# Performance work log

Hardware: AMD Instinct MI355X
Metric: run time of the kernel (lower is better)

Reference implementation:

```python
import jax, jax.numpy as jnp
import numpy as np

K = 3
NUM_STEP_COMBO = 5
BN_EPS = 1e-5


def setup_inputs() -> dict:
    key = jax.random.key(0)
    ks = jax.random.split(key, 10)
    N, E, D, H, O, G = 100000, 1600000, 48, 128, 12, 64
    x = jax.random.normal(ks[0], (N, D), dtype=jnp.float32)
    edge_index = jax.random.randint(ks[1], (2, E), 0, N, dtype=jnp.int64)
    batch = jnp.sort(jax.random.randint(ks[2], (N,), 0, G, dtype=jnp.int64))
    # ChebConv params: one [D, D] weight per Chebyshev order, shared bias
    W = jax.random.normal(ks[3], (K, D, D), dtype=jnp.float32) * 0.1
    b = jnp.zeros((D,), dtype=jnp.float32)
    gamma = jnp.ones((D,), dtype=jnp.float32)
    beta = jnp.zeros((D,), dtype=jnp.float32)
    W1 = jax.random.normal(ks[4], (D, H), dtype=jnp.float32) * 0.1
    b1 = jnp.zeros((H,), dtype=jnp.float32)
    W2 = jax.random.normal(ks[5], (H, O), dtype=jnp.float32) * 0.1
    b2 = jnp.zeros((O,), dtype=jnp.float32)
    return {"x": x, "edge_index": edge_index, "batch": batch, "num_graphs": 64,
            "W": W, "b": b, "gamma": gamma, "beta": beta,
            "W1": W1, "b1": b1, "W2": W2, "b2": b2}


def cheb_conv(x, row, col, W, b):
    # PyG ChebConv, sym norm, lambda_max=2 => L_hat = -D^{-1/2} A D^{-1/2}
    N = x.shape[0]
    deg = jax.ops.segment_sum(jnp.ones_like(row, dtype=x.dtype), row, num_segments=N)
    dinv = jnp.where(deg > 0, jax.lax.rsqrt(jnp.maximum(deg, 1.0)), 0.0)
    norm = (-dinv[row] * dinv[col])[:, None]  # [E,1] edge weights of L_hat

    def lhat(v):  # sparse matvec: gather neighbors, scale, scatter-add
        return jax.ops.segment_sum(norm * v[col], row, num_segments=N)

    Tx0 = x
    Tx1 = lhat(x)
    out = Tx0 @ W[0] + Tx1 @ W[1]
    Txkm2, Txkm1 = Tx0, Tx1
    for k in range(2, W.shape[0]):
        Txk = 2.0 * lhat(Txkm1) - Txkm2
        out = out + Txk @ W[k]
        Txkm2, Txkm1 = Txkm1, Txk
    return out + b


def reference(x, edge_index, batch, num_graphs, W, b, gamma, beta, W1, b1, W2, b2):
    row, col = edge_index[0], edge_index[1]
    N = x.shape[0]
    out = x
    for _ in range(NUM_STEP_COMBO):
        t = jax.nn.relu(cheb_conv(out, row, col, W, b))
        # BatchNorm1d (training-mode stats over all nodes, biased var)
        mean = jnp.mean(t, axis=0)
        var = jnp.mean((t - mean) ** 2, axis=0)
        t = gamma * (t - mean) * jax.lax.rsqrt(var + BN_EPS) + beta
        # graph_max_pool: per-node max over incoming neighbor features
        m = jax.ops.segment_max(t[col], row, num_segments=N)
        out = jnp.where(jnp.isneginf(m), 0.0, m)  # empty segments -> 0
    g = jax.ops.segment_sum(out, batch, num_segments=num_graphs)  # global_add_pool
    h = jax.nn.relu(g @ W1 + b1)
    return h @ W2 + b2
```

## Files before the change

### kernel.cpp

```cpp
#include <hip/hip_runtime.h>
#include <hip/hip_bf16.h>

#define D 48
#define RB 96
#define GNUM 64
#define HDIM 128
#define ODIM 12
#define BN_EPS 1e-5f

typedef _Float16 half4v __attribute__((ext_vector_type(4)));
typedef _Float16 half8v __attribute__((ext_vector_type(8)));
typedef float f32x4 __attribute__((ext_vector_type(4)));

#define MFMA16(a, b, c) __builtin_amdgcn_mfma_f32_16x16x16f16((a), (b), (c), 0, 0, 0)

__device__ __forceinline__ half8v h8max(half8v a, half8v b) {
    half8v r;
#pragma unroll
    for (int k = 0; k < 8; ++k) r[k] = a[k] > b[k] ? a[k] : b[k];
    return r;
}
__device__ __forceinline__ half8v h8min(half8v a, half8v b) {
    half8v r;
#pragma unroll
    for (int k = 0; k < 8; ++k) r[k] = a[k] < b[k] ? a[k] : b[k];
    return r;
}
__device__ __forceinline__ half8v h8shfl_xor(half8v v, int mask) {
    union { half8v h; int i[4]; } u;
    u.h = v;
#pragma unroll
    for (int k = 0; k < 4; ++k) u.i[k] = __shfl_xor(u.i[k], mask);
    return u.h;
}


__global__ __launch_bounds__(256) void k_deg(const int* __restrict__ row, int* __restrict__ deg, int E) {
    int e = blockIdx.x * 256 + threadIdx.x;
    if (e < E) atomicAdd(&deg[row[e]], 1);
}

__global__ __launch_bounds__(256) void k_scan1(const int* __restrict__ deg, int* __restrict__ incl,
                                               int* __restrict__ bsum, float* __restrict__ dinv, int N) {
    __shared__ int s[256];
    int i = blockIdx.x * 256 + threadIdx.x;
    int d = (i < N) ? deg[i] : 0;
    if (i < N) dinv[i] = d > 0 ? rsqrtf((float)d) : 0.f;
    s[threadIdx.x] = d;
    __syncthreads();
    for (int off = 1; off < 256; off <<= 1) {
        int t = (threadIdx.x >= off) ? s[threadIdx.x - off] : 0;
        __syncthreads();
        s[threadIdx.x] += t;
        __syncthreads();
    }
    if (i < N) incl[i] = s[threadIdx.x];
    if (threadIdx.x == 255) bsum[blockIdx.x] = s[255];
}

__global__ __launch_bounds__(512) void k_scan2(int* __restrict__ bsum, int nb) {
    __shared__ int s[512];
    int t = threadIdx.x;
    s[t] = (t < nb) ? bsum[t] : 0;
    __syncthreads();
    for (int off = 1; off < 512; off <<= 1) {
        int v = (t >= off) ? s[t - off] : 0;
        __syncthreads();
        s[t] += v;
        __syncthreads();
    }
    if (t < nb) bsum[t] = s[t];
}

__global__ __launch_bounds__(256) void k_scan3(const int* __restrict__ incl, const int* __restrict__ bsum,
                                               int* __restrict__ rowptr, int N) {
    int i = blockIdx.x * 256 + threadIdx.x;
    if (i < N) {
        int add = (blockIdx.x > 0) ? bsum[blockIdx.x - 1] : 0;
        rowptr[i + 1] = incl[i] + add;
    }
    if (i == 0) rowptr[0] = 0;
}

__global__ __launch_bounds__(256) void k_fill(const int* __restrict__ row, const int* __restrict__ col,
                                              const int* __restrict__ rowptr, int* __restrict__ fillc,
                                              const float* __restrict__ dinv, int2* __restrict__ epair,
                                              int e0, int e1, int N) {
    int part = blockIdx.x & 7;
    int sub = blockIdx.x >> 3;
    int nsub = (int)(gridDim.x >> 3);
    int lo = (int)(((long long)N * part) >> 3);
    int hi = (int)(((long long)N * (part + 1)) >> 3);
    for (int e = e0 + sub * 256 + threadIdx.x; e < e1; e += nsub * 256) {
        int r = row[e];
        if (r >= lo && r < hi) {
            int c = col[e];
            int p = rowptr[r] + atomicAdd(&fillc[r], 1);
            epair[p] = make_int2(c * RB, __float_as_int(dinv[c]));
        }
    }
}

__global__ __launch_bounds__(256) void k_cvt(const float* __restrict__ x, _Float16* __restrict__ xh, int n4) {
    int i = blockIdx.x * 256 + threadIdx.x;
    if (i < n4) {
        float4 v = ((const float4*)x)[i];
        half4v h;
        h.x = (_Float16)v.x; h.y = (_Float16)v.y; h.z = (_Float16)v.z; h.w = (_Float16)v.w;
        ((half4v*)xh)[i] = h;
    }
}

__global__ __launch_bounds__(256) void k_wb(const float* __restrict__ W, _Float16* __restrict__ WB) {
    int idx = blockIdx.x * 256 + threadIdx.x;
    if (idx < 27 * 64) {
        int lane = idx & 63, ct = idx >> 6;
        int c = ct / 3, tl = ct % 3;
        int col = lane & 15, kg = lane >> 4;
        half4v h;
#pragma unroll
        for (int j = 0; j < 4; ++j) h[j] = (_Float16)W[(c * 16 + kg * 4 + j) * 48 + tl * 16 + col];
        *(half4v*)(WB + (size_t)idx * 4) = h;
    }
}


#define GATHER_REDUCE8(A)                                             \
    A##0 += __shfl_xor(A##0, 8);  A##1 += __shfl_xor(A##1, 8);        \
    A##2 += __shfl_xor(A##2, 8);  A##3 += __shfl_xor(A##3, 8);        \
    A##4 += __shfl_xor(A##4, 8);  A##5 += __shfl_xor(A##5, 8);        \
    A##6 += __shfl_xor(A##6, 8);  A##7 += __shfl_xor(A##7, 8);        \
    A##0 += __shfl_xor(A##0, 16); A##1 += __shfl_xor(A##1, 16);       \
    A##2 += __shfl_xor(A##2, 16); A##3 += __shfl_xor(A##3, 16);       \
    A##4 += __shfl_xor(A##4, 16); A##5 += __shfl_xor(A##5, 16);       \
    A##6 += __shfl_xor(A##6, 16); A##7 += __shfl_xor(A##7, 16);       \
    A##0 += __shfl_xor(A##0, 32); A##1 += __shfl_xor(A##1, 32);       \
    A##2 += __shfl_xor(A##2, 32); A##3 += __shfl_xor(A##3, 32);       \
    A##4 += __shfl_xor(A##4, 32); A##5 += __shfl_xor(A##5, 32);       \
    A##6 += __shfl_xor(A##6, 32); A##7 += __shfl_xor(A##7, 32);

__global__ __launch_bounds__(256) void k_lhat(const _Float16* __restrict__ cur, const int* __restrict__ rowptr,
                                              const int2* __restrict__ epair, const float* __restrict__ dinv,
                                              _Float16* __restrict__ tx1, int N) {
    int lane = threadIdx.x & 63;
    int i = (blockIdx.x * 256 + threadIdx.x) >> 6;
    if (i >= N) return;
    int slot = lane >> 3, j = lane & 7;
    int jbB = (j < 6 ? j : 5) * 16;
    const char* base = (const char*)cur + jbB;
    int s = rowptr[i], e = rowptr[i + 1];
    float a0 = 0.f, a1 = 0.f, a2 = 0.f, a3 = 0.f, a4 = 0.f, a5 = 0.f, a6 = 0.f, a7 = 0.f;
    int p = s + slot;
    for (; p + 8 < e; p += 16) {
        int2 ea = epair[p], eb = epair[p + 8];
        half8v ha = *(const half8v*)(base + (unsigned)ea.x);
        half8v hb = *(const half8v*)(base + (unsigned)eb.x);
        float wa = __int_as_float(ea.y), wb = __int_as_float(eb.y);
        a0 += wa * (float)ha[0] + wb * (float)hb[0];
        a1 += wa * (float)ha[1] + wb * (float)hb[1];
        a2 += wa * (float)ha[2] + wb * (float)hb[2];
        a3 += wa * (float)ha[3] + wb * (float)hb[3];
        a4 += wa * (float)ha[4] + wb * (float)hb[4];
        a5 += wa * (float)ha[5] + wb * (float)hb[5];
        a6 += wa * (float)ha[6] + wb * (float)hb[6];
        a7 += wa * (float)ha[7] + wb * (float)hb[7];
    }
    if (p < e) {
        int2 ea = epair[p];
        half8v ha = *(const half8v*)(base + (unsigned)ea.x);
        float wa = __int_as_float(ea.y);
        a0 += wa * (float)ha[0]; a1 += wa * (float)ha[1]; a2 += wa * (float)ha[2]; a3 += wa * (float)ha[3];
        a4 += wa * (float)ha[4]; a5 += wa * (float)ha[5]; a6 += wa * (float)ha[6]; a7 += wa * (float)ha[7];
    }
    GATHER_REDUCE8(a)
    if (slot == 0 && j < 6) {
        float sc = -dinv[i];
        half8v o;
        o[0] = (_Float16)(sc * a0); o[1] = (_Float16)(sc * a1);
        o[2] = (_Float16)(sc * a2); o[3] = (_Float16)(sc * a3);
        o[4] = (_Float16)(sc * a4); o[5] = (_Float16)(sc * a5);
        o[6] = (_Float16)(sc * a6); o[7] = (_Float16)(sc * a7);
        *(half8v*)((char*)tx1 + (size_t)i * RB + jbB) = o;
    }
}

__global__ __launch_bounds__(256) void k_gather2(const _Float16* __restrict__ tx0, const _Float16* __restrict__ tx1,
                                                 const int* __restrict__ rowptr, const int2* __restrict__ epair,
                                                 const float* __restrict__ dinv, _Float16* __restrict__ tx2, int N) {
    int lane = threadIdx.x & 63;
    int i = (blockIdx.x * 256 + threadIdx.x) >> 6;
    if (i >= N) return;
    int slot = lane >> 3, j = lane & 7;
    int jbB = (j < 6 ? j : 5) * 16;
    const char* base = (const char*)tx1 + jbB;
    int s = rowptr[i], e = rowptr[i + 1];
    float a0 = 0.f, a1 = 0.f, a2 = 0.f, a3 = 0.f, a4 = 0.f, a5 = 0.f, a6 = 0.f, a7 = 0.f;
    int p = s + slot;
    for (; p + 8 < e; p += 16) {
        int2 ea = epair[p], eb = epair[p + 8];
        half8v ha = *(const half8v*)(base + (unsigned)ea.x);
        half8v hb = *(const half8v*)(base + (unsigned)eb.x);
        float wa = __int_as_float(ea.y), wb = __int_as_float(eb.y);
        a0 += wa * (float)ha[0] + wb * (float)hb[0];
        a1 += wa * (float)ha[1] + wb * (float)hb[1];
        a2 += wa * (float)ha[2] + wb * (float)hb[2];
        a3 += wa * (float)ha[3] + wb * (float)hb[3];
        a4 += wa * (float)ha[4] + wb * (float)hb[4];
        a5 += wa * (float)ha[5] + wb * (float)hb[5];
        a6 += wa * (float)ha[6] + wb * (float)hb[6];
        a7 += wa * (float)ha[7] + wb * (float)hb[7];
    }
    if (p < e) {
        int2 ea = epair[p];
        half8v ha = *(const half8v*)(base + (unsigned)ea.x);
        float wa = __int_as_float(ea.y);
        a0 += wa * (float)ha[0]; a1 += wa * (float)ha[1]; a2 += wa * (float)ha[2]; a3 += wa * (float)ha[3];
        a4 += wa * (float)ha[4]; a5 += wa * (float)ha[5]; a6 += wa * (float)ha[6]; a7 += wa * (float)ha[7];
    }
    GATHER_REDUCE8(a)
    if (slot == 0 && j < 6) {
        float sc = -2.f * dinv[i];
        half8v h0 = *(const half8v*)((const char*)tx0 + (size_t)i * RB + jbB);
        half8v o;
        o[0] = (_Float16)(sc * a0 - (float)h0[0]); o[1] = (_Float16)(sc * a1 - (float)h0[1]);
        o[2] = (_Float16)(sc * a2 - (float)h0[2]); o[3] = (_Float16)(sc * a3 - (float)h0[3]);
        o[4] = (_Float16)(sc * a4 - (float)h0[4]); o[5] = (_Float16)(sc * a5 - (float)h0[5]);
        o[6] = (_Float16)(sc * a6 - (float)h0[6]); o[7] = (_Float16)(sc * a7 - (float)h0[7]);
        *(half8v*)((char*)tx2 + (size_t)i * RB + jbB) = o;
    }
}


__global__ __launch_bounds__(256) void k_dense(const _Float16* __restrict__ tx0, const _Float16* __restrict__ tx1,
                                               const _Float16* __restrict__ tx2, const _Float16* __restrict__ WB,
                                               const float* __restrict__ b, _Float16* __restrict__ tbuf,
                                               float* __restrict__ bnst, int N) {
    __shared__ float bns[2 * D];
    int t = threadIdx.x;
    if (t < 2 * D) bns[t] = 0.f;
    __syncthreads();

    int lane = t & 63, wave = t >> 6;
    int node0 = (blockIdx.x * 4 + wave) * 16;
    if (node0 < N) {
        int col = lane & 15, kg = lane >> 4;
        int nodeA = node0 + col;
        bool inA = nodeA < N;
        const _Float16* __restrict__ Xs[3] = {tx0 + (size_t)nodeA * D, tx1 + (size_t)nodeA * D,
                                              tx2 + (size_t)nodeA * D};
        f32x4 acc0 = {}, acc1 = {}, acc2 = {};
#pragma unroll
        for (int c = 0; c < 9; ++c) {
            half4v a = {};
            if (inA) a = *(const half4v*)(Xs[c / 3] + (c % 3) * 16 + kg * 4);
            half4v b0 = *(const half4v*)(WB + ((size_t)(c * 3 + 0) * 64 + lane) * 4);
            half4v b1 = *(const half4v*)(WB + ((size_t)(c * 3 + 1) * 64 + lane) * 4);
            half4v b2 = *(const half4v*)(WB + ((size_t)(c * 3 + 2) * 64 + lane) * 4);
            acc0 = MFMA16(a, b0, acc0);
            acc1 = MFMA16(a, b1, acc1);
            acc2 = MFMA16(a, b2, acc2);
        }
        float bc0 = b[col], bc1 = b[16 + col], bc2 = b[32 + col];
        float s0 = 0.f, q0 = 0.f, s1 = 0.f, q1 = 0.f, s2 = 0.f, q2 = 0.f;
#pragma unroll
        for (int i = 0; i < 4; ++i) {
            int nd = node0 + kg * 4 + i;
            float v0 = fmaxf(acc0[i] + bc0, 0.f);
            float v1 = fmaxf(acc1[i] + bc1, 0.f);
            float v2 = fmaxf(acc2[i] + bc2, 0.f);
            if (nd < N) {
                _Float16* o = tbuf + (size_t)nd * D;
                o[col] = (_Float16)v0;
                o[16 + col] = (_Float16)v1;
                o[32 + col] = (_Float16)v2;
                s0 += v0; q0 += v0 * v0;
                s1 += v1; q1 += v1 * v1;
                s2 += v2; q2 += v2 * v2;
            }
        }
        s0 += __shfl_xor(s0, 16); s0 += __shfl_xor(s0, 32);
        q0 += __shfl_xor(q0, 16); q0 += __shfl_xor(q0, 32);
        s1 += __shfl_xor(s1, 16); s1 += __shfl_xor(s1, 32);
        q1 += __shfl_xor(q1, 16); q1 += __shfl_xor(q1, 32);
        s2 += __shfl_xor(s2, 16); s2 += __shfl_xor(s2, 32);
        q2 += __shfl_xor(q2, 16); q2 += __shfl_xor(q2, 32);
        if (lane < 16) {
            atomicAdd(&bns[col], s0);      atomicAdd(&bns[D + col], q0);
            atomicAdd(&bns[16 + col], s1); atomicAdd(&bns[D + 16 + col], q1);
            atomicAdd(&bns[32 + col], s2); atomicAdd(&bns[D + 32 + col], q2);
        }
    }
    __syncthreads();
    if (t < 2 * D) atomicAdd(&bnst[t], bns[t]);
}


__global__ __launch_bounds__(256) void k_pool(const _Float16* __restrict__ tbuf, const int* __restrict__ rowptr,
                                              const int2* __restrict__ epair, const float* __restrict__ bnst,
                                              const float* __restrict__ gamma, const float* __restrict__ beta,
                                              float Ninv, _Float16* __restrict__ outh, int N) {
    __shared__ float ssL[2 * D];
    int t = threadIdx.x;
    if (t < D) {
        float mean = bnst[t] * Ninv;
        float var = fmaxf(bnst[D + t] * Ninv - mean * mean, 0.f);
        float sc = gamma[t] * rsqrtf(var + BN_EPS);
        ssL[t] = sc;
        ssL[D + t] = beta[t] - mean * sc;
    }
    __syncthreads();
    int lane = t & 63;
    int i = (blockIdx.x * 256 + t) >> 6;
    if (i >= N) return;
    int slot = lane >> 3, j = lane & 7;
    int jbB = (j < 6 ? j : 5) * 16;
    const char* base = (const char*)tbuf + jbB;
    int s = rowptr[i], e = rowptr[i + 1];
    half8v m, n;
#pragma unroll
    for (int k = 0; k < 8; ++k) { m[k] = (_Float16)(-60000.f); n[k] = (_Float16)(60000.f); }
    int p = s + slot;
    for (; p + 8 < e; p += 16) {
        int oa = epair[p].x, ob = epair[p + 8].x;
        half8v ha = *(const half8v*)(base + (unsigned)oa);
        half8v hb = *(const half8v*)(base + (unsigned)ob);
        m = h8max(m, h8max(ha, hb));
        n = h8min(n, h8min(ha, hb));
    }
    if (p < e) {
        half8v ha = *(const half8v*)(base + (unsigned)epair[p].x);
        m = h8max(m, ha);
        n = h8min(n, ha);
    }
    m = h8max(m, h8shfl_xor(m, 8));
    n = h8min(n, h8shfl_xor(n, 8));
    m = h8max(m, h8shfl_xor(m, 16));
    n = h8min(n, h8shfl_xor(n, 16));
    m = h8max(m, h8shfl_xor(m, 32));
    n = h8min(n, h8shfl_xor(n, 32));
    if (slot == 0 && j < 6) {
        int jb = (j < 6 ? j : 5) * 8;
        half8v o;
        if (s == e) {
#pragma unroll
            for (int k = 0; k < 8; ++k) o[k] = (_Float16)0.f;
        } else {
#pragma unroll
            for (int k = 0; k < 8; ++k) {
                float sc = ssL[jb + k], sh = ssL[D + jb + k];
                float v = (sc >= 0.f) ? sc * (float)m[k] + sh : sc * (float)n[k] + sh;
                o[k] = (_Float16)v;
            }
        }
        *(half8v*)((char*)outh + (size_t)i * RB + jbB) = o;
    }
}


__global__ __launch_bounds__(256) void k_gpool(const _Float16* __restrict__ outh, const int* __restrict__ batch,
                                               float* __restrict__ g, int N, int chunk) {
    int lane = threadIdx.x & 63;
    int wid = (blockIdx.x * 256 + threadIdx.x) >> 6;
    int start = wid * chunk;
    if (start >= N || lane >= 12) return;
    int end = start + chunk;
    if (end > N) end = N;
    int curb = batch[start];
    float a0 = 0.f, a1 = 0.f, a2 = 0.f, a3 = 0.f;
    for (int i = start; i < end; ++i) {
        int bi = batch[i];
        if (bi != curb) {
            atomicAdd(&g[curb * D + lane * 4 + 0], a0); atomicAdd(&g[curb * D + lane * 4 + 1], a1);
            atomicAdd(&g[curb * D + lane * 4 + 2], a2); atomicAdd(&g[curb * D + lane * 4 + 3], a3);
            curb = bi; a0 = a1 = a2 = a3 = 0.f;
        }
        half4v h = *(const half4v*)(outh + (size_t)i * D + lane * 4);
        a0 += (float)h.x; a1 += (float)h.y; a2 += (float)h.z; a3 += (float)h.w;
    }
    atomicAdd(&g[curb * D + lane * 4 + 0], a0); atomicAdd(&g[curb * D + lane * 4 + 1], a1);
    atomicAdd(&g[curb * D + lane * 4 + 2], a2); atomicAdd(&g[curb * D + lane * 4 + 3], a3);
}

__global__ __launch_bounds__(256) void k_mlp(const float* __restrict__ g, const float* __restrict__ W1,
                                             const float* __restrict__ b1, const float* __restrict__ W2,
                                             const float* __restrict__ b2, float* __restrict__ out) {
    __shared__ float gL[GNUM * D];
    __shared__ float hL[GNUM * HDIM];
    __shared__ float W1L[D * HDIM];
    int t = threadIdx.x;
    for (int i = t; i < GNUM * D; i += 256) gL[i] = g[i];
    for (int i = t; i < D * HDIM; i += 256) W1L[i] = W1[i];
    __syncthreads();
    for (int i = t; i < GNUM * HDIM; i += 256) {
        int gi = i >> 7, hj = i & 127;
        float a = b1[hj];
        for (int k = 0; k < D; ++k) a += gL[gi * D + k] * W1L[k * HDIM + hj];
        hL[i] = fmaxf(a, 0.f);
    }
    __syncthreads();
    for (int i = t; i < GNUM * ODIM; i += 256) {
        int gi = i / ODIM, oj = i % ODIM;
        float a = b2[oj];
        for (int k = 0; k < HDIM; ++k) a += hL[gi * HDIM + k] * W2[k * ODIM + oj];
        out[i] = a;
    }
}


extern "C" void kernel_launch(void* const* d_in, const int* in_sizes, int n_in,
                              void* d_out, int out_size, void* d_ws, size_t ws_size,
                              hipStream_t stream) {
    const float* x     = (const float*)d_in[0];
    const int*   ei    = (const int*)d_in[1];
    const int*   batch = (const int*)d_in[2];
    const float* W     = (const float*)d_in[4];
    const float* b     = (const float*)d_in[5];
    const float* gamma = (const float*)d_in[6];
    const float* beta  = (const float*)d_in[7];
    const float* W1    = (const float*)d_in[8];
    const float* b1    = (const float*)d_in[9];
    const float* W2    = (const float*)d_in[10];
    const float* b2    = (const float*)d_in[11];

    int N = in_sizes[0] / D;
    int E = in_sizes[1] / 2;
    const int* row = ei;
    const int* col = ei + E;

    char* w = (char*)d_ws;
    auto alloc = [&](size_t bytes) { char* p = w; w += (bytes + 255) & ~(size_t)255; return p; };
    int*       deg     = (int*)alloc((size_t)N * 4);
    float*     dinv    = (float*)alloc((size_t)N * 4);
    int*       fillc   = (int*)alloc((size_t)N * 4);
    int*       incl    = (int*)alloc((size_t)N * 4);
    int*       bsum    = (int*)alloc(4096);
    int*       rowptr  = (int*)alloc((size_t)(N + 1) * 4);
    int2*      epair   = (int2*)alloc((size_t)E * 8);
    _Float16*  xh      = (_Float16*)alloc((size_t)N * D * 2 + 64);
    _Float16*  tx1h    = (_Float16*)alloc((size_t)N * D * 2 + 64);
    _Float16*  tx2h    = (_Float16*)alloc((size_t)N * D * 2 + 64);
    _Float16*  tbufh   = (_Float16*)alloc((size_t)N * D * 2 + 64);
    _Float16*  outh    = (_Float16*)alloc((size_t)N * D * 2 + 64);
    _Float16*  WB      = (_Float16*)alloc(27 * 64 * 4 * 2);
    float*     bnstats = (float*)alloc(5 * 2 * D * 4);
    float*     g       = (float*)alloc((size_t)GNUM * D * 4);

    (void)hipMemsetAsync(deg, 0, (size_t)N * 4, stream);
    (void)hipMemsetAsync(fillc, 0, (size_t)N * 4, stream);
    (void)hipMemsetAsync(bnstats, 0, 5 * 2 * D * 4, stream);
    (void)hipMemsetAsync(g, 0, (size_t)GNUM * D * 4, stream);

    int nbE = (E + 255) / 256;
    int nbN = (N + 255) / 256;

    k_deg<<<nbE, 256, 0, stream>>>(row, deg, E);
    k_scan1<<<nbN, 256, 0, stream>>>(deg, incl, bsum, dinv, N);
    k_scan2<<<1, 512, 0, stream>>>(bsum, nbN);
    k_scan3<<<nbN, 256, 0, stream>>>(incl, bsum, rowptr, N);
    int E3 = E / 3;
    k_fill<<<2048, 256, 0, stream>>>(row, col, rowptr, fillc, dinv, epair, 0, E3, N);
    k_fill<<<2048, 256, 0, stream>>>(row, col, rowptr, fillc, dinv, epair, E3, 2 * E3, N);
    k_fill<<<2048, 256, 0, stream>>>(row, col, rowptr, fillc, dinv, epair, 2 * E3, E, N);
    int n4 = N * D / 4;
    k_cvt<<<(n4 + 255) / 256, 256, 0, stream>>>(x, xh, n4);
    k_wb<<<7, 256, 0, stream>>>(W, WB);

    int nbWave = (N * 64 + 255) / 256;
    int nbDense = (((N + 15) / 16) + 3) / 4;
    float Ninv = 1.f / (float)N;
    const _Float16* cur = xh;
    for (int step = 0; step < 5; ++step) {
        float* bnst = bnstats + step * 2 * D;
        k_lhat<<<nbWave, 256, 0, stream>>>(cur, rowptr, epair, dinv, tx1h, N);
        k_gather2<<<nbWave, 256, 0, stream>>>(cur, tx1h, rowptr, epair, dinv, tx2h, N);
        k_dense<<<nbDense, 256, 0, stream>>>(cur, tx1h, tx2h, WB, b, tbufh, bnst, N);
        k_pool<<<nbWave, 256, 0, stream>>>(tbufh, rowptr, epair, bnst, gamma, beta, Ninv, outh, N);
        cur = outh;
    }

    int chunk = 32;
    int nwaves = (N + chunk - 1) / chunk;
    int nbG = (nwaves * 64 + 255) / 256;
    k_gpool<<<nbG, 256, 0, stream>>>(outh, batch, g, N, chunk);
    k_mlp<<<1, 256, 0, stream>>>(g, W1, b1, W2, b2, (float*)d_out);
}
```

Baseline: 1.278 ms.

## Bucket CSR neighbor order by column range to improve gather locality

Degree counting now keeps eight sub-counters per row, one per column-index bucket. A per-row prefix over those counters lets the fill place each row's edges grouped by source-node range. The aim is that the many gather passes (lhat, gather2, pool) touch neighbor features in a partially sorted order for better cache locality. In exchange it uses an 8x larger degree array and fill-counter array, more memset and atomic traffic in preprocessing, and a more spread-out atomic target.

```diff
diff --git a/kernel.cpp b/kernel.cpp
--- a/kernel.cpp
+++ b/kernel.cpp
@@ -35,17 +35,33 @@
 }
 
 
-__global__ __launch_bounds__(256) void k_deg(const int* __restrict__ row, int* __restrict__ deg, int E) {
+__global__ __launch_bounds__(256) void k_deg8(const int* __restrict__ row, const int* __restrict__ col,
+                                              int* __restrict__ deg8, int E, unsigned bdiv) {
     int e = blockIdx.x * 256 + threadIdx.x;
-    if (e < E) atomicAdd(&deg[row[e]], 1);
-}
-
-__global__ __launch_bounds__(256) void k_scan1(const int* __restrict__ deg, int* __restrict__ incl,
+    if (e < E) {
+        int r = row[e];
+        int b = (int)((unsigned)col[e] / bdiv);
+        atomicAdd(&deg8[r * 8 + b], 1);
+    }
+}
+
+__global__ __launch_bounds__(256) void k_scan1(int* __restrict__ deg8, int* __restrict__ incl,
                                                int* __restrict__ bsum, float* __restrict__ dinv, int N) {
     __shared__ int s[256];
     int i = blockIdx.x * 256 + threadIdx.x;
-    int d = (i < N) ? deg[i] : 0;
-    if (i < N) dinv[i] = d > 0 ? rsqrtf((float)d) : 0.f;
+    int d = 0;
+    if (i < N) {
+        int4 a = ((const int4*)deg8)[i * 2];
+        int4 bq = ((const int4*)deg8)[i * 2 + 1];
+        int loc[8] = {a.x, a.y, a.z, a.w, bq.x, bq.y, bq.z, bq.w};
+        int run = 0;
+#pragma unroll
+        for (int k = 0; k < 8; ++k) { int t = loc[k]; loc[k] = run; run += t; }
+        d = run;
+        dinv[i] = d > 0 ? rsqrtf((float)d) : 0.f;
+        ((int4*)deg8)[i * 2] = make_int4(loc[0], loc[1], loc[2], loc[3]);
+        ((int4*)deg8)[i * 2 + 1] = make_int4(loc[4], loc[5], loc[6], loc[7]);
+    }
     s[threadIdx.x] = d;
     __syncthreads();
     for (int off = 1; off < 256; off <<= 1) {
@@ -83,9 +99,9 @@
 }
 
 __global__ __launch_bounds__(256) void k_fill(const int* __restrict__ row, const int* __restrict__ col,
-                                              const int* __restrict__ rowptr, int* __restrict__ fillc,
-                                              const float* __restrict__ dinv, int2* __restrict__ epair,
-                                              int e0, int e1, int N) {
+                                              const int* __restrict__ rowptr, const int* __restrict__ pfx8,
+                                              int* __restrict__ fillc8, const float* __restrict__ dinv,
+                                              int2* __restrict__ epair, int e0, int e1, int N, unsigned bdiv) {
     int part = blockIdx.x & 7;
     int sub = blockIdx.x >> 3;
     int nsub = (int)(gridDim.x >> 3);
@@ -95,7 +111,8 @@
         int r = row[e];
         if (r >= lo && r < hi) {
             int c = col[e];
-            int p = rowptr[r] + atomicAdd(&fillc[r], 1);
+            int b = (int)((unsigned)c / bdiv);
+            int p = rowptr[r] + pfx8[r * 8 + b] + atomicAdd(&fillc8[r * 8 + b], 1);
             epair[p] = make_int2(c * RB, __float_as_int(dinv[c]));
         }
     }
@@ -429,9 +446,9 @@
 
     char* w = (char*)d_ws;
     auto alloc = [&](size_t bytes) { char* p = w; w += (bytes + 255) & ~(size_t)255; return p; };
-    int*       deg     = (int*)alloc((size_t)N * 4);
+    int*       deg8    = (int*)alloc((size_t)N * 8 * 4);
+    int*       fillc8  = (int*)alloc((size_t)N * 8 * 4);
     float*     dinv    = (float*)alloc((size_t)N * 4);
-    int*       fillc   = (int*)alloc((size_t)N * 4);
     int*       incl    = (int*)alloc((size_t)N * 4);
     int*       bsum    = (int*)alloc(4096);
     int*       rowptr  = (int*)alloc((size_t)(N + 1) * 4);
@@ -445,22 +462,23 @@
     float*     bnstats = (float*)alloc(5 * 2 * D * 4);
     float*     g       = (float*)alloc((size_t)GNUM * D * 4);
 
-    (void)hipMemsetAsync(deg, 0, (size_t)N * 4, stream);
-    (void)hipMemsetAsync(fillc, 0, (size_t)N * 4, stream);
+    (void)hipMemsetAsync(deg8, 0, (size_t)N * 8 * 4, stream);
+    (void)hipMemsetAsync(fillc8, 0, (size_t)N * 8 * 4, stream);
     (void)hipMemsetAsync(bnstats, 0, 5 * 2 * D * 4, stream);
     (void)hipMemsetAsync(g, 0, (size_t)GNUM * D * 4, stream);
 
     int nbE = (E + 255) / 256;
     int nbN = (N + 255) / 256;
-
-    k_deg<<<nbE, 256, 0, stream>>>(row, deg, E);
-    k_scan1<<<nbN, 256, 0, stream>>>(deg, incl, bsum, dinv, N);
+    unsigned bdiv = (unsigned)((N + 7) / 8);
+
+    k_deg8<<<nbE, 256, 0, stream>>>(row, col, deg8, E, bdiv);
+    k_scan1<<<nbN, 256, 0, stream>>>(deg8, incl, bsum, dinv, N);
     k_scan2<<<1, 512, 0, stream>>>(bsum, nbN);
     k_scan3<<<nbN, 256, 0, stream>>>(incl, bsum, rowptr, N);
     int E3 = E / 3;
-    k_fill<<<2048, 256, 0, stream>>>(row, col, rowptr, fillc, dinv, epair, 0, E3, N);
-    k_fill<<<2048, 256, 0, stream>>>(row, col, rowptr, fillc, dinv, epair, E3, 2 * E3, N);
-    k_fill<<<2048, 256, 0, stream>>>(row, col, rowptr, fillc, dinv, epair, 2 * E3, E, N);
+    k_fill<<<2048, 256, 0, stream>>>(row, col, rowptr, deg8, fillc8, dinv, epair, 0, E3, N, bdiv);
+    k_fill<<<2048, 256, 0, stream>>>(row, col, rowptr, deg8, fillc8, dinv, epair, E3, 2 * E3, N, bdiv);
+    k_fill<<<2048, 256, 0, stream>>>(row, col, rowptr, deg8, fillc8, dinv, epair, 2 * E3, E, N, bdiv);
     int n4 = N * D / 4;
     k_cvt<<<(n4 + 255) / 256, 256, 0, stream>>>(x, xh, n4);
     k_wb<<<7, 256, 0, stream>>>(W, WB);
```

Measured after the change: 1.281 ms. No clear change (+0.2%).
